# Optimization experiments

Hardware: AMD Instinct MI355X
Metric: run time of the kernel (lower is better)

Reference implementation:

```python
import jax, jax.numpy as jnp
import numpy as np

A, T, N_GRID, RBF, F = 128, 2048, 65536, 16, 128
L_DIMS = (1, 3, 5)  # irreps 0e, 1e, 2e


def setup_inputs() -> dict:
    key = jax.random.key(0)
    ks = jax.random.split(key, 16)
    nrm = lambda k, s, sc=1.0: jax.random.normal(k, s, dtype=jnp.float32) * sc
    w_sc = 1.0 / np.sqrt(F).astype(np.float32)
    return {
        "feat0": nrm(ks[0], (A, F, 1)),
        "feat1": nrm(ks[1], (A, F, 3)),
        "feat2": nrm(ks[2], (A, F, 5)),
        "sph0": nrm(ks[3], (A, T, 1)),
        "sph1": nrm(ks[4], (A, T, 3)),
        "sph2": nrm(ks[5], (A, T, 5)),
        "radial_basis_vals": jax.random.uniform(ks[6], (A, T, RBF), dtype=jnp.float32),
        "mlp_w1": nrm(ks[7], (3, F, F), w_sc),
        "mlp_b1": jnp.zeros((3, F), jnp.float32),
        "mlp_w2": nrm(ks[8], (3, F, F), w_sc),
        "mlp_b2": jnp.zeros((3, F), jnp.float32),
        "mlp_w3": nrm(ks[9], (3, F, RBF * F), w_sc),
        "mlp_b3": jnp.zeros((3, RBF * F), jnp.float32),
        "truncated_idx": jax.random.randint(ks[10], (T,), 0, N_GRID, dtype=jnp.int32),
        "N": N_GRID,
    }


def reference(feat0, feat1, feat2, sph0, sph1, sph2, radial_basis_vals,
              mlp_w1, mlp_b1, mlp_w2, mlp_b2, mlp_w3, mlp_b3,
              truncated_idx, N):
    f_dim = feat0.shape[1]
    rbf = radial_basis_vals.shape[-1]
    inv_features = feat0[..., 0]  # (A, F) scalar (0e) channel
    inv_rbf = jnp.asarray(1.0 / np.sqrt(rbf), dtype=feat0.dtype)
    feats = (feat0, feat1, feat2)
    sphs = (sph0, sph1, sph2)
    spatial_features = jnp.zeros((N, f_dim), dtype=feat0.dtype)
    for i in range(3):  # fixed small loop over irrep chunks
        h = jax.nn.silu(inv_features @ mlp_w1[i] + mlp_b1[i])
        h = jax.nn.silu(h @ mlp_w2[i] + mlp_b2[i])
        rbf_to_f = (h @ mlp_w3[i] + mlp_b3[i]).reshape(-1, rbf, f_dim) * inv_rbf  # (A, RBF, F)
        # reduce over atoms n, sph index d, radial index r -> (T, F)
        sparse = jnp.einsum('ntd,nfd,ntr,nrf->tf', sphs[i], feats[i],
                            radial_basis_vals, rbf_to_f)
        spatial_features = spatial_features.at[truncated_idx].add(sparse)
    return spatial_features
```

## Files before the change

### kernel.cpp

```cpp
#include <hip/hip_runtime.h>
#include <hip/hip_bf16.h>
#include <cstdint>
#include <cstddef>

#define A_DIM 128
#define T_DIM 2048
#define F_DIM 128
#define RBF_DIM 16
#define KDD 2048
#define VT_LD 18432
#define NKG 16
#define NA 8
#define BT 32

typedef __attribute__((ext_vector_type(8))) short short8;
typedef __attribute__((ext_vector_type(4))) float f32x4;
typedef __attribute__((ext_vector_type(4))) unsigned int u32x4;

__device__ __forceinline__ float silu_f(float x) {
    return x / (1.0f + __expf(-x));
}

__device__ __forceinline__ unsigned short f2bf(float x) {
    union { float f; unsigned u; } v; v.f = x;
    unsigned r = v.u + 0x7FFFu + ((v.u >> 16) & 1u);
    return (unsigned short)(r >> 16);
}

__device__ __forceinline__ void gl_lds16(const void* g, void* l) {
    __builtin_amdgcn_global_load_lds(
        (const __attribute__((address_space(1))) void*)g,
        (__attribute__((address_space(3))) void*)l, 16, 0, 0);
}

__global__ void zero_kernel(float4* __restrict__ p, int n4) {
    const int stride = gridDim.x * blockDim.x;
    const float4 z = {0.f, 0.f, 0.f, 0.f};
    for (int i = blockIdx.x * blockDim.x + threadIdx.x; i < n4; i += stride)
        p[i] = z;
}

__global__ void mlp_fused_kernel(const float* __restrict__ feat0,
                                 const float* __restrict__ w1, const float* __restrict__ b1,
                                 const float* __restrict__ w2, const float* __restrict__ b2,
                                 const float* __restrict__ w3, const float* __restrict__ b3,
                                 float* __restrict__ rbfws) {
    __shared__ float inv_s[4 * F_DIM];
    __shared__ float h_s[4 * F_DIM];
    __shared__ float h2_s[4 * F_DIM];
    const int i  = blockIdx.y;
    const int a0 = blockIdx.x * 4;
    const int tid = threadIdx.x;
    const int f  = tid & 127;
    const int la = tid >> 7;

    inv_s[tid] = feat0[(a0 + la) * F_DIM + f];
    __syncthreads();

    const float* w1i = w1 + (size_t)i * F_DIM * F_DIM;
    float x = b1[i * F_DIM + f];
    #pragma unroll 8
    for (int k = 0; k < F_DIM; ++k)
        x = fmaf(inv_s[la * F_DIM + k], w1i[k * F_DIM + f], x);
    h_s[tid] = silu_f(x);
    __syncthreads();

    const float* w2i = w2 + (size_t)i * F_DIM * F_DIM;
    float y = b2[i * F_DIM + f];
    #pragma unroll 8
    for (int k = 0; k < F_DIM; ++k)
        y = fmaf(h_s[la * F_DIM + k], w2i[k * F_DIM + f], y);
    h2_s[tid] = silu_f(y);
    __syncthreads();

    const int c = tid * 4;
    const float* w3i = w3 + (size_t)i * F_DIM * 2048;
    float val[4][4];
    #pragma unroll
    for (int a = 0; a < 4; ++a) {
        #pragma unroll
        for (int cc = 0; cc < 4; ++cc)
            val[a][cc] = b3[i * 2048 + c + cc];
    }
    for (int k = 0; k < F_DIM; ++k) {
        const float4 w = *reinterpret_cast<const float4*>(&w3i[(size_t)k * 2048 + c]);
        #pragma unroll
        for (int a = 0; a < 4; ++a) {
            const float h = h2_s[a * F_DIM + k];
            val[a][0] = fmaf(h, w.x, val[a][0]);
            val[a][1] = fmaf(h, w.y, val[a][1]);
            val[a][2] = fmaf(h, w.z, val[a][2]);
            val[a][3] = fmaf(h, w.w, val[a][3]);
        }
    }
    const float inv_rbf = 0.25f;
    #pragma unroll
    for (int a = 0; a < 4; ++a) {
        float4 o;
        o.x = val[a][0] * inv_rbf;
        o.y = val[a][1] * inv_rbf;
        o.z = val[a][2] * inv_rbf;
        o.w = val[a][3] * inv_rbf;
        *reinterpret_cast<float4*>(&rbfws[((size_t)i * A_DIM + a0 + a) * 2048 + c]) = o;
    }
}

__global__ void build_vt_kernel(const float* __restrict__ feat0,
                                const float* __restrict__ feat1,
                                const float* __restrict__ feat2,
                                const float* __restrict__ rbfws,
                                unsigned short* __restrict__ Vt) {
    const int n  = blockIdx.x;
    const int dd = blockIdx.y;
    const int f  = threadIdx.x;

    int i, d;
    float fv;
    if (dd == 0)      { i = 0; d = 0;      fv = feat0[n * F_DIM + f]; }
    else if (dd < 4)  { i = 1; d = dd - 1; fv = feat1[(n * F_DIM + f) * 3 + d]; }
    else              { i = 2; d = dd - 4; fv = feat2[(n * F_DIM + f) * 5 + d]; }

    const float* rb = rbfws + ((size_t)(i * A_DIM + n) * RBF_DIM) * F_DIM + f;
    unsigned short* vp = Vt + (size_t)f * VT_LD + (size_t)dd * KDD + n * 16;
    #pragma unroll
    for (int r = 0; r < RBF_DIM; ++r)
        vp[r] = f2bf(fv * rb[(size_t)r * F_DIM]);
}

template<int MODE>
__global__ void __launch_bounds__(256) gemm_kernel(
        const float* __restrict__ sph0, const float* __restrict__ sph1,
        const float* __restrict__ sph2, const float* __restrict__ radial,
        const unsigned short* __restrict__ Vt,
        float* __restrict__ outbuf,
        float* __restrict__ dout, int out_n4) {
    __shared__ unsigned short b_s[F_DIM * 128];
    __shared__ float sph_s[NA * BT];

    const int tid  = threadIdx.x;
    const int lane = tid & 63;
    const int w    = tid >> 6;
    const int wr   = w >> 1;
    const int wc   = w & 1;
    const int t0   = blockIdx.x * BT + wr * 16;
    const int n0   = blockIdx.y * NA;
    const int kq   = lane >> 4;
    const int lf   = lane & 15;

    if (MODE == 0) {
        const int bid = blockIdx.y * gridDim.x + blockIdx.x;
        const float4 z = {0.f, 0.f, 0.f, 0.f};
        float4* zp = (float4*)dout;
        #pragma unroll
        for (int q = 0; q < 8; ++q) {
            const int idx = bid * 2048 + q * 256 + tid;
            if (idx < out_n4) zp[idx] = z;
        }
    }

    f32x4 rad[4][2];
    #pragma unroll
    for (int ks = 0; ks < 4; ++ks) {
        const int n = n0 + 2 * ks + (kq >> 1);
        const int t = t0 + lf;
        const float* rp = radial + ((size_t)n * T_DIM + t) * 16 + (kq & 1) * 8;
        rad[ks][0] = *reinterpret_cast<const f32x4*>(rp);
        rad[ks][1] = *reinterpret_cast<const f32x4*>(rp + 4);
    }

    const int fs_row = tid >> 4;
    const int cs     = (tid & 15) ^ ((tid >> 4) & 7);
    const unsigned short* gsrc0 = Vt + (size_t)fs_row * VT_LD + n0 * 16 + cs * 8;
    const int nn_s = tid >> 5;
    const int tt_s = tid & 31;
    const size_t sph_tbase = (size_t)(n0 + nn_s) * T_DIM + blockIdx.x * BT + tt_s;

    f32x4 acc[4];
    #pragma unroll
    for (int nf = 0; nf < 4; ++nf)
        acc[nf] = (f32x4){0.f, 0.f, 0.f, 0.f};

    #pragma unroll 1
    for (int dd = 0; dd < 9; ++dd) {
        const float* sp; int smul, soff;
        if (dd == 0)     { sp = sph0; smul = 1; soff = 0; }
        else if (dd < 4) { sp = sph1; smul = 3; soff = dd - 1; }
        else             { sp = sph2; smul = 5; soff = dd - 4; }

        __syncthreads();

        const size_t koff = (size_t)dd * KDD;
        #pragma unroll
        for (int q = 0; q < 8; ++q) {
            const unsigned short* gp = gsrc0 + koff + (size_t)(q * 16) * VT_LD;
            void* lp = (void*)((char*)b_s + q * 4096 + w * 1024);
            gl_lds16(gp, lp);
        }
        sph_s[tid] = sp[sph_tbase * smul + soff];

        __syncthreads();

        #pragma unroll
        for (int ks = 0; ks < 4; ++ks) {
            short8 bfr[4];
            #pragma unroll
            for (int nf = 0; nf < 4; ++nf) {
                const int f = wc * 64 + 16 * nf + lf;
                const int byte = f * 256 + (((ks * 4 + kq) ^ (lf & 7)) * 16);
                bfr[nf] = *reinterpret_cast<const short8*>((const char*)b_s + byte);
            }
            const float s = sph_s[(2 * ks + (kq >> 1)) * BT + wr * 16 + lf];
            unsigned int d0, d1, d2, d3;
            asm("v_cvt_pk_bf16_f32 %0, %1, %2" : "=v"(d0)
                : "v"(s * rad[ks][0][0]), "v"(s * rad[ks][0][1]));
            asm("v_cvt_pk_bf16_f32 %0, %1, %2" : "=v"(d1)
                : "v"(s * rad[ks][0][2]), "v"(s * rad[ks][0][3]));
            asm("v_cvt_pk_bf16_f32 %0, %1, %2" : "=v"(d2)
                : "v"(s * rad[ks][1][0]), "v"(s * rad[ks][1][1]));
            asm("v_cvt_pk_bf16_f32 %0, %1, %2" : "=v"(d3)
                : "v"(s * rad[ks][1][2]), "v"(s * rad[ks][1][3]));
            union { u32x4 u; short8 s8; } au;
            au.u = (u32x4){d0, d1, d2, d3};
            #pragma unroll
            for (int nf = 0; nf < 4; ++nf)
                acc[nf] = __builtin_amdgcn_mfma_f32_16x16x32_bf16(
                    au.s8, bfr[nf], acc[nf], 0, 0, 0);
        }
    }

    float* pb = (MODE == 0)
        ? outbuf + (size_t)blockIdx.y * (T_DIM * F_DIM)
        : outbuf;
    #pragma unroll
    for (int nf = 0; nf < 4; ++nf) {
        const int f = wc * 64 + 16 * nf + lf;
        #pragma unroll
        for (int reg = 0; reg < 4; ++reg) {
            const int t = t0 + 4 * kq + reg;
            if (MODE == 0)
                pb[(size_t)t * F_DIM + f] = acc[nf][reg];
            else
                atomicAdd(&pb[(size_t)t * F_DIM + f], acc[nf][reg]);
        }
    }
}

__global__ void scatter_sum_kernel(const float* __restrict__ partial,
                                   const int* __restrict__ tidx,
                                   float* __restrict__ out) {
    const int tid = threadIdx.x;
    const int t = blockIdx.x * 2 + (tid >> 7);
    const int f = tid & 127;
    const int g = tidx[t];
    const float* p = partial + (size_t)t * F_DIM + f;
    float s = 0.0f;
    #pragma unroll
    for (int kg = 0; kg < NKG; ++kg)
        s += p[(size_t)kg * (T_DIM * F_DIM)];
    atomicAdd(&out[(size_t)g * F_DIM + f], s);
}

__global__ void scatter_kernel(const float* __restrict__ sparse,
                               const int* __restrict__ tidx,
                               float* __restrict__ out) {
    const int tid = threadIdx.x;
    const int t = blockIdx.x * 2 + (tid >> 7);
    const int f = tid & 127;
    const int g = tidx[t];
    atomicAdd(&out[(size_t)g * F_DIM + f], sparse[(size_t)t * F_DIM + f]);
}

extern "C" void kernel_launch(void* const* d_in, const int* in_sizes, int n_in,
                              void* d_out, int out_size, void* d_ws, size_t ws_size,
                              hipStream_t stream) {
    const float* feat0  = (const float*)d_in[0];
    const float* feat1  = (const float*)d_in[1];
    const float* feat2  = (const float*)d_in[2];
    const float* sph0   = (const float*)d_in[3];
    const float* sph1   = (const float*)d_in[4];
    const float* sph2   = (const float*)d_in[5];
    const float* radial = (const float*)d_in[6];
    const float* w1     = (const float*)d_in[7];
    const float* b1     = (const float*)d_in[8];
    const float* w2     = (const float*)d_in[9];
    const float* b2     = (const float*)d_in[10];
    const float* w3     = (const float*)d_in[11];
    const float* b3     = (const float*)d_in[12];
    const int*   tidx   = (const int*)d_in[13];
    float* out = (float*)d_out;

    float* rbfws  = (float*)d_ws;
    float* h2ws   = rbfws + 3 * A_DIM * RBF_DIM * F_DIM;

    const size_t plain_need =
        (size_t)(3 * A_DIM * RBF_DIM * F_DIM + 3 * A_DIM * F_DIM) * sizeof(float) +
        (size_t)F_DIM * VT_LD * sizeof(unsigned short) +
        (size_t)NKG * T_DIM * F_DIM * sizeof(float);
    const bool plain = (ws_size >= plain_need);

    mlp_fused_kernel<<<dim3(A_DIM / 4, 3), 512, 0, stream>>>(
        feat0, w1, b1, w2, b2, w3, b3, rbfws);

    if (plain) {
        unsigned short* Vt = (unsigned short*)(h2ws + 3 * A_DIM * F_DIM);
        float* partial = (float*)(Vt + (size_t)F_DIM * VT_LD);
        build_vt_kernel<<<dim3(A_DIM, 9), 128, 0, stream>>>(feat0, feat1, feat2, rbfws, Vt);
        gemm_kernel<0><<<dim3(T_DIM / BT, A_DIM / NA), 256, 0, stream>>>(
            sph0, sph1, sph2, radial, Vt, partial, out, out_size / 4);
        scatter_sum_kernel<<<dim3(T_DIM / 2), 256, 0, stream>>>(partial, tidx, out);
    } else {
        float* sparse = h2ws + 3 * A_DIM * F_DIM;
        unsigned short* Vt = (unsigned short*)(sparse + T_DIM * F_DIM);
        zero_kernel<<<2048, 256, 0, stream>>>((float4*)out, out_size / 4);
        hipMemsetAsync(sparse, 0, (size_t)T_DIM * F_DIM * sizeof(float), stream);
        build_vt_kernel<<<dim3(A_DIM, 9), 128, 0, stream>>>(feat0, feat1, feat2, rbfws, Vt);
        gemm_kernel<1><<<dim3(T_DIM / BT, A_DIM / NA), 256, 0, stream>>>(
            sph0, sph1, sph2, radial, Vt, sparse, out, out_size / 4);
        scatter_kernel<<<dim3(T_DIM / 2), 256, 0, stream>>>(sparse, tidx, out);
    }
}
```

Before: 64.63 us.

## Fuse split-K reduction and scatter into GEMM tail via last-block counters

The separate scatter_sum kernel is removed. Each GEMM block now increments a per-T-tile counter, and the last of the 16 atom-group blocks sums the partials and does the atomic scatter into the output. Zeroing of the output moves from the GEMM prologue into the MLP kernel, and the counters are reset in build_vt. This saves a kernel launch and the zeroing work inside the GEMM. In exchange it adds threadfences and a serialized reduction tail on the last-arriving block of each tile.

After: 192.7 us. 198% more time.

```diff
diff --git a/kernel.cpp b/kernel.cpp
--- a/kernel.cpp
+++ b/kernel.cpp
@@ -12,6 +12,7 @@
 #define NKG 16
 #define NA 8
 #define BT 32
+#define NMT (T_DIM / BT)
 
 typedef __attribute__((ext_vector_type(8))) short short8;
 typedef __attribute__((ext_vector_type(4))) float f32x4;
@@ -44,7 +45,8 @@
                                  const float* __restrict__ w1, const float* __restrict__ b1,
                                  const float* __restrict__ w2, const float* __restrict__ b2,
                                  const float* __restrict__ w3, const float* __restrict__ b3,
-                                 float* __restrict__ rbfws) {
+                                 float* __restrict__ rbfws,
+                                 float4* __restrict__ outz, int out_n4) {
     __shared__ float inv_s[4 * F_DIM];
     __shared__ float h_s[4 * F_DIM];
     __shared__ float h2_s[4 * F_DIM];
@@ -54,6 +56,14 @@
     const int f  = tid & 127;
     const int la = tid >> 7;
 
+    {
+        const int gstride = gridDim.x * gridDim.y * 512;
+        const int gtid = (blockIdx.y * gridDim.x + blockIdx.x) * 512 + tid;
+        const float4 z = {0.f, 0.f, 0.f, 0.f};
+        for (int idx = gtid; idx < out_n4; idx += gstride)
+            outz[idx] = z;
+    }
+
     inv_s[tid] = feat0[(a0 + la) * F_DIM + f];
     __syncthreads();
 
@@ -109,10 +119,13 @@
                                 const float* __restrict__ feat1,
                                 const float* __restrict__ feat2,
                                 const float* __restrict__ rbfws,
-                                unsigned short* __restrict__ Vt) {
+                                unsigned short* __restrict__ Vt,
+                                int* __restrict__ counters) {
     const int n  = blockIdx.x;
     const int dd = blockIdx.y;
     const int f  = threadIdx.x;
+
+    if (n == 0 && dd == 0 && f < NMT) counters[f] = 0;
 
     int i, d;
     float fv;
@@ -133,9 +146,12 @@
         const float* __restrict__ sph2, const float* __restrict__ radial,
         const unsigned short* __restrict__ Vt,
         float* __restrict__ outbuf,
-        float* __restrict__ dout, int out_n4) {
+        int* __restrict__ counters,
+        const int* __restrict__ tidx,
+        float* __restrict__ out) {
     __shared__ unsigned short b_s[F_DIM * 128];
     __shared__ float sph_s[NA * BT];
+    __shared__ int is_last;
 
     const int tid  = threadIdx.x;
     const int lane = tid & 63;
@@ -146,17 +162,6 @@
     const int n0   = blockIdx.y * NA;
     const int kq   = lane >> 4;
     const int lf   = lane & 15;
-
-    if (MODE == 0) {
-        const int bid = blockIdx.y * gridDim.x + blockIdx.x;
-        const float4 z = {0.f, 0.f, 0.f, 0.f};
-        float4* zp = (float4*)dout;
-        #pragma unroll
-        for (int q = 0; q < 8; ++q) {
-            const int idx = bid * 2048 + q * 256 + tid;
-            if (idx < out_n4) zp[idx] = z;
-        }
-    }
 
     f32x4 rad[4][2];
     #pragma unroll
@@ -243,21 +248,39 @@
                 atomicAdd(&pb[(size_t)t * F_DIM + f], acc[nf][reg]);
         }
     }
-}
-
-__global__ void scatter_sum_kernel(const float* __restrict__ partial,
-                                   const int* __restrict__ tidx,
-                                   float* __restrict__ out) {
-    const int tid = threadIdx.x;
-    const int t = blockIdx.x * 2 + (tid >> 7);
-    const int f = tid & 127;
-    const int g = tidx[t];
-    const float* p = partial + (size_t)t * F_DIM + f;
-    float s = 0.0f;
-    #pragma unroll
-    for (int kg = 0; kg < NKG; ++kg)
-        s += p[(size_t)kg * (T_DIM * F_DIM)];
-    atomicAdd(&out[(size_t)g * F_DIM + f], s);
+
+    if (MODE == 0) {
+        __threadfence();
+        __syncthreads();
+        if (tid == 0) {
+            const int prev = atomicAdd(&counters[blockIdx.x], 1);
+            is_last = (prev == NKG - 1);
+        }
+        __syncthreads();
+        if (is_last) {
+            __threadfence();
+            #pragma unroll
+            for (int q = 0; q < 4; ++q) {
+                const int item = q * 256 + tid;
+                const int tt   = item >> 5;
+                const int c4   = item & 31;
+                const int t    = blockIdx.x * BT + tt;
+                const float4* pp = (const float4*)outbuf + (size_t)t * 32 + c4;
+                float4 s = {0.f, 0.f, 0.f, 0.f};
+                #pragma unroll
+                for (int kg = 0; kg < NKG; ++kg) {
+                    const float4 v = pp[(size_t)kg * (T_DIM * 32)];
+                    s.x += v.x; s.y += v.y; s.z += v.z; s.w += v.w;
+                }
+                const int g = tidx[t];
+                float* op = out + (size_t)g * F_DIM + c4 * 4;
+                atomicAdd(op + 0, s.x);
+                atomicAdd(op + 1, s.y);
+                atomicAdd(op + 2, s.z);
+                atomicAdd(op + 3, s.w);
+            }
+        }
+    }
 }
 
 __global__ void scatter_kernel(const float* __restrict__ sparse,
@@ -295,27 +318,30 @@
     const size_t plain_need =
         (size_t)(3 * A_DIM * RBF_DIM * F_DIM + 3 * A_DIM * F_DIM) * sizeof(float) +
         (size_t)F_DIM * VT_LD * sizeof(unsigned short) +
-        (size_t)NKG * T_DIM * F_DIM * sizeof(float);
+        (size_t)NKG * T_DIM * F_DIM * sizeof(float) + NMT * sizeof(int);
     const bool plain = (ws_size >= plain_need);
 
     mlp_fused_kernel<<<dim3(A_DIM / 4, 3), 512, 0, stream>>>(
-        feat0, w1, b1, w2, b2, w3, b3, rbfws);
+        feat0, w1, b1, w2, b2, w3, b3, rbfws, (float4*)out, out_size / 4);
 
     if (plain) {
         unsigned short* Vt = (unsigned short*)(h2ws + 3 * A_DIM * F_DIM);
         float* partial = (float*)(Vt + (size_t)F_DIM * VT_LD);
-        build_vt_kernel<<<dim3(A_DIM, 9), 128, 0, stream>>>(feat0, feat1, feat2, rbfws, Vt);
+        int* counters  = (int*)(partial + (size_t)NKG * T_DIM * F_DIM);
+        build_vt_kernel<<<dim3(A_DIM, 9), 128, 0, stream>>>(
+            feat0, feat1, feat2, rbfws, Vt, counters);
         gemm_kernel<0><<<dim3(T_DIM / BT, A_DIM / NA), 256, 0, stream>>>(
-            sph0, sph1, sph2, radial, Vt, partial, out, out_size / 4);
-        scatter_sum_kernel<<<dim3(T_DIM / 2), 256, 0, stream>>>(partial, tidx, out);
+            sph0, sph1, sph2, radial, Vt, partial, counters, tidx, out);
     } else {
         float* sparse = h2ws + 3 * A_DIM * F_DIM;
         unsigned short* Vt = (unsigned short*)(sparse + T_DIM * F_DIM);
+        int* counters = (int*)(Vt + (size_t)F_DIM * VT_LD);
         zero_kernel<<<2048, 256, 0, stream>>>((float4*)out, out_size / 4);
         hipMemsetAsync(sparse, 0, (size_t)T_DIM * F_DIM * sizeof(float), stream);
-        build_vt_kernel<<<dim3(A_DIM, 9), 128, 0, stream>>>(feat0, feat1, feat2, rbfws, Vt);
+        build_vt_kernel<<<dim3(A_DIM, 9), 128, 0, stream>>>(
+            feat0, feat1, feat2, rbfws, Vt, counters);
         gemm_kernel<1><<<dim3(T_DIM / BT, A_DIM / NA), 256, 0, stream>>>(
-            sph0, sph1, sph2, radial, Vt, sparse, out, out_size / 4);
+            sph0, sph1, sph2, radial, Vt, sparse, counters, tidx, out);
         scatter_kernel<<<dim3(T_DIM / 2), 256, 0, stream>>>(sparse, tidx, out);
     }
 }
```
